# Kernel tuning notes

Measured on AMD Instinct MI355X. Metric: run time of the kernel, lower is better.

The kernel has to match this reference:

```python
import jax, jax.numpy as jnp
import numpy as np

B, T, D, U = 32, 2048, 512, 512


def setup_inputs() -> dict:
    key = jax.random.key(0)
    ks = jax.random.split(key, 6)
    value = jax.random.normal(ks[0], (B, T, D), dtype=jnp.float32)
    query = jax.random.normal(ks[1], (B, D), dtype=jnp.float32)
    mask = jax.random.randint(ks[2], (B, T), 0, 2, dtype=jnp.int32)
    # Glorot-ish scaled dense weights (no bias, matching Dense(use_bias=False))
    W1 = jax.random.normal(ks[3], (D, U), dtype=jnp.float32) * (1.0 / np.sqrt(D))
    W2 = jax.random.normal(ks[4], (D, U), dtype=jnp.float32) * (1.0 / np.sqrt(D))
    V = jax.random.normal(ks[5], (U,), dtype=jnp.float32) * (1.0 / np.sqrt(U))
    return {"value": value, "query": query, "mask": mask, "W1": W1, "W2": W2, "V": V}


def reference(value, query, mask, W1, W2, V):
    # Additive (Bahdanau) attention scores: u[b,t] = V . tanh(value[b,t] @ W1 + query[b] @ W2)
    w1_key = jnp.einsum('btd,du->btu', value, W1)          # [B, T, U]
    w2_query = jnp.einsum('bd,du->bu', query, W2)          # [B, U]
    u = jnp.einsum('btu,u->bt', jnp.tanh(w1_key + w2_query[:, None, :]), V)  # [B, T]
    # Masking: add -1e20 where mask == 0 (same as keras reference)
    u = u + (1.0 - mask.astype(u.dtype)) * jnp.asarray(-1e20, dtype=u.dtype)
    a = jax.nn.softmax(u, axis=1)                          # [B, T]
    # Pointer extraction: gather value row at argmax of attention weights
    idx = jnp.argmax(a, axis=1)                            # [B]
    context = jnp.take_along_axis(value, idx[:, None, None], axis=1)[:, 0, :]  # [B, D]
    return (context, a)
```

## Files before the change

### kernel.cpp

```cpp
#include <hip/hip_runtime.h>
#include <hip/hip_bf16.h>
#include <hip/hip_fp16.h>
#include <stdint.h>

#define B_ 32
#define T_ 2048
#define D_ 512
#define U_ 512
#define M_ (B_ * T_)

#define BM 64
#define BK 32
#define SAW 520
#define MAXC 4

typedef _Float16 half8  __attribute__((ext_vector_type(8)));
typedef float   floatx4 __attribute__((ext_vector_type(4)));

__device__ __forceinline__ float tanh_fast(float x) {
    float ax = fabsf(x);
    float e  = __expf(2.0f * ax);
    float t  = 1.0f - 2.0f / (e + 1.0f);
    return copysignf(t, x);
}

__device__ __forceinline__ void gld_lds16(const void* gsrc, void* lds_dst) {
    typedef __attribute__((address_space(1))) const char gch;
    typedef __attribute__((address_space(3))) char lch;
    __builtin_amdgcn_global_load_lds((const gch*)(uintptr_t)gsrc,
                                     (lch*)(uint32_t)(uintptr_t)lds_dst,
                                     16, 0, 0);
}

__global__ __launch_bounds__(256)
void k_prep(const float* __restrict__ W1, const float* __restrict__ query,
            const float* __restrict__ W2, _Float16* __restrict__ W1T,
            float* __restrict__ w2q) {
    const int bid = blockIdx.x;
    const int tid = threadIdx.x;
    if (bid < 64) {
        __shared__ float tile[64][65];
        const int bx = bid & 7;
        const int by = bid >> 3;
        const int k0 = bx * 64, n0 = by * 64;
        const int tx = tid & 63;
        const int ty = tid >> 6;
#pragma unroll
        for (int i = 0; i < 16; ++i) {
            int r = ty * 16 + i;
            tile[r][tx] = W1[(size_t)(k0 + r) * U_ + n0 + tx];
        }
        __syncthreads();
#pragma unroll
        for (int i = 0; i < 16; ++i) {
            int r = ty * 16 + i;
            W1T[(size_t)(n0 + r) * D_ + k0 + tx] = (_Float16)tile[tx][r];
        }
    } else {
        __shared__ float sq[D_];
        __shared__ float part[128];
        const int id = bid - 64;
        const int b  = id >> 2;
        const int nq = id & 3;
        sq[tid]       = query[b * D_ + tid];
        sq[tid + 256] = query[b * D_ + tid + 256];
        __syncthreads();
        const int n  = nq * 128 + (tid & 127);
        const int dh = tid >> 7;
        float acc = 0.f;
        const int d0 = dh * 256;
#pragma unroll 16
        for (int d = d0; d < d0 + 256; ++d)
            acc = fmaf(sq[d], W2[(size_t)d * U_ + n], acc);
        if (dh == 1) part[tid & 127] = acc;
        __syncthreads();
        if (dh == 0) w2q[b * U_ + n] = acc + part[tid];
    }
}

__global__ __launch_bounds__(512)
void k_gemm_u(const float* __restrict__ value,
              const _Float16* __restrict__ W1T,
              const float* __restrict__ w2q,
              const float* __restrict__ Vv,
              float* __restrict__ u_out) {
    __shared__ __align__(16) _Float16 sA[BM * SAW];
    __shared__ __align__(16) _Float16 sB[2][U_ * BK];
    __shared__ float sW2q[U_];
    __shared__ float sV[U_];
    __shared__ float sRed[8][BM];

    const int tid  = threadIdx.x;
    const int wave = tid >> 6;
    const int lane = tid & 63;
    const int l15  = lane & 15;
    const int lg   = lane >> 4;
    const int m0   = blockIdx.x * BM;
    const int b    = m0 >> 11;

    sW2q[tid] = w2q[b * U_ + tid];
    sV[tid]   = Vv[tid];

    const int bn  = lane >> 2;
    const int bk8 = (lane & 3) * 8;

#pragma unroll
    for (int jj = 0; jj < 4; ++jj) {
        const int inst = wave * 4 + jj;
        const int n = inst * 16 + bn;
        gld_lds16(W1T + (size_t)n * D_ + bk8, (void*)(&sB[0][inst * 512]));
    }

#pragma unroll
    for (int j = 0; j < 8; ++j) {
        const int row = wave * 8 + j;
        const float* src = value + (size_t)(m0 + row) * D_ + lane * 8;
        const floatx4 x0 = *(const floatx4*)(src);
        const floatx4 x1 = *(const floatx4*)(src + 4);
        half8 h;
        h[0] = (_Float16)x0[0]; h[1] = (_Float16)x0[1];
        h[2] = (_Float16)x0[2]; h[3] = (_Float16)x0[3];
        h[4] = (_Float16)x1[0]; h[5] = (_Float16)x1[1];
        h[6] = (_Float16)x1[2]; h[7] = (_Float16)x1[3];
        *(half8*)(&sA[row * SAW + lane * 8]) = h;
    }

    floatx4 acc[4][4];
    const floatx4 zero4 = {0.f, 0.f, 0.f, 0.f};
#pragma unroll
    for (int i = 0; i < 4; ++i)
#pragma unroll
        for (int j = 0; j < 4; ++j) acc[i][j] = zero4;

    __syncthreads();

    for (int kk = 0; kk < 16; ++kk) {
        const int cur = kk & 1;
        if (kk < 15) {
            const int k0n = (kk + 1) * BK;
#pragma unroll
            for (int jj = 0; jj < 4; ++jj) {
                const int inst = wave * 4 + jj;
                const int n = inst * 16 + bn;
                gld_lds16(W1T + (size_t)n * D_ + k0n + bk8,
                          (void*)(&sB[cur ^ 1][inst * 512]));
            }
        }
        half8 af[4], bf[4];
#pragma unroll
        for (int mi = 0; mi < 4; ++mi)
            af[mi] = *(const half8*)(&sA[(mi * 16 + l15) * SAW + kk * BK + lg * 8]);
#pragma unroll
        for (int ni = 0; ni < 4; ++ni) {
            const int n = wave * 64 + ni * 16 + l15;
            bf[ni] = *(const half8*)(&sB[cur][n * BK + lg * 8]);
        }
#pragma unroll
        for (int ni = 0; ni < 4; ++ni)
#pragma unroll
            for (int mi = 0; mi < 4; ++mi)
                acc[mi][ni] = __builtin_amdgcn_mfma_f32_16x16x32_f16(
                    af[mi], bf[ni], acc[mi][ni], 0, 0, 0);
        __syncthreads();
    }

    float ps[4][4];
#pragma unroll
    for (int mi = 0; mi < 4; ++mi)
#pragma unroll
        for (int j = 0; j < 4; ++j) ps[mi][j] = 0.f;

#pragma unroll
    for (int ni = 0; ni < 4; ++ni) {
        const int n = wave * 64 + ni * 16 + l15;
        const float w2 = sW2q[n];
        const float vv = sV[n];
#pragma unroll
        for (int mi = 0; mi < 4; ++mi)
#pragma unroll
            for (int j = 0; j < 4; ++j)
                ps[mi][j] += vv * tanh_fast(acc[mi][ni][j] + w2);
    }
#pragma unroll
    for (int off = 1; off < 16; off <<= 1)
#pragma unroll
        for (int mi = 0; mi < 4; ++mi)
#pragma unroll
            for (int j = 0; j < 4; ++j)
                ps[mi][j] += __shfl_xor(ps[mi][j], off, 64);

    if (l15 == 0) {
#pragma unroll
        for (int mi = 0; mi < 4; ++mi)
#pragma unroll
            for (int j = 0; j < 4; ++j)
                sRed[wave][mi * 16 + lg * 4 + j] = ps[mi][j];
    }
    __syncthreads();
    if (tid < BM) {
        float s = 0.f;
#pragma unroll
        for (int w = 0; w < 8; ++w) s += sRed[w][tid];
        u_out[m0 + tid] = s;
    }
}

__global__ __launch_bounds__(256)
void k_post(const float* __restrict__ u, const int* __restrict__ mask,
            const float* __restrict__ value, const float* __restrict__ W1,
            const float* __restrict__ w2q, const float* __restrict__ Vv,
            float* __restrict__ a_out, float* __restrict__ ctx_out) {
    __shared__ float sx[T_];
    __shared__ float rv[4];
    __shared__ int   ri[4];
    __shared__ float s_scalar;
    __shared__ int   s_cand[MAXC];
    __shared__ float s_score[MAXC];
    __shared__ __align__(16) float vrows[MAXC][D_];
    __shared__ int   s_t;

    const int b = blockIdx.x;
    const int tid = threadIdx.x;
    const int wave = tid >> 6, lane = tid & 63;

#pragma unroll
    for (int i = 0; i < 8; ++i) {
        const int t = tid * 8 + i;
        float x = u[b * T_ + t];
        if (mask[b * T_ + t] == 0) x = -1e20f;
        sx[t] = x;
    }
    __syncthreads();

    for (int r = 0; r < MAXC; ++r) {
        float v = -INFINITY; int vi = 0;
#pragma unroll
        for (int i = 0; i < 8; ++i) {
            const int t = tid * 8 + i;
            const float x = sx[t];
            if (x > v) { v = x; vi = t; }
        }
        for (int off = 32; off > 0; off >>= 1) {
            const float ov = __shfl_down(v, off, 64);
            const int   oi = __shfl_down(vi, off, 64);
            if (ov > v || (ov == v && oi < vi)) { v = ov; vi = oi; }
        }
        if (lane == 0) { rv[wave] = v; ri[wave] = vi; }
        __syncthreads();
        if (tid == 0) {
            float bv = rv[0]; int bi = ri[0];
            for (int w = 1; w < 4; ++w)
                if (rv[w] > bv || (rv[w] == bv && ri[w] < bi)) { bv = rv[w]; bi = ri[w]; }
            s_cand[r] = bi;
            if (r == 0) s_scalar = bv;
            sx[bi] = -INFINITY;
        }
        __syncthreads();
    }
    const float mx = s_scalar;

    float zloc = 0.f;
    float evals[8];
#pragma unroll
    for (int i = 0; i < 8; ++i) {
        const int t = tid * 8 + i;
        float x = u[b * T_ + t];
        if (mask[b * T_ + t] == 0) x = -1e20f;
        const float e = __expf(x - mx);
        evals[i] = e;
        zloc += e;
    }
    for (int off = 32; off > 0; off >>= 1) zloc += __shfl_down(zloc, off, 64);
    if (lane == 0) rv[wave] = zloc;
    __syncthreads();
    if (tid == 0) s_scalar = 1.0f / (rv[0] + rv[1] + rv[2] + rv[3]);
    __syncthreads();
    const float rz = s_scalar;
#pragma unroll
    for (int i = 0; i < 8; ++i) {
        const int t = tid * 8 + i;
        a_out[b * T_ + t] = evals[i] * rz;
    }

#pragma unroll
    for (int ci = 0; ci < MAXC; ++ci) {
        const int t = s_cand[ci];
        vrows[ci][tid]       = value[((size_t)b * T_ + t) * D_ + tid];
        vrows[ci][tid + 256] = value[((size_t)b * T_ + t) * D_ + tid + 256];
    }
    __syncthreads();

    float dots[2][MAXC];
#pragma unroll
    for (int j = 0; j < 2; ++j)
#pragma unroll
        for (int ci = 0; ci < MAXC; ++ci) dots[j][ci] = 0.f;

    for (int d4 = 0; d4 < D_; d4 += 4) {
        floatx4 vr[MAXC];
#pragma unroll
        for (int ci = 0; ci < MAXC; ++ci)
            vr[ci] = *(const floatx4*)(&vrows[ci][d4]);
#pragma unroll
        for (int k = 0; k < 4; ++k) {
            const float w0 = W1[(size_t)(d4 + k) * U_ + tid];
            const float w1 = W1[(size_t)(d4 + k) * U_ + tid + 256];
#pragma unroll
            for (int ci = 0; ci < MAXC; ++ci) {
                dots[0][ci] = fmaf(vr[ci][k], w0, dots[0][ci]);
                dots[1][ci] = fmaf(vr[ci][k], w1, dots[1][ci]);
            }
        }
    }
    float sc[MAXC];
#pragma unroll
    for (int ci = 0; ci < MAXC; ++ci) {
        const float n0v = Vv[tid]       * tanhf(dots[0][ci] + w2q[b * U_ + tid]);
        const float n1v = Vv[tid + 256] * tanhf(dots[1][ci] + w2q[b * U_ + tid + 256]);
        sc[ci] = n0v + n1v;
    }
#pragma unroll
    for (int ci = 0; ci < MAXC; ++ci)
        for (int off = 32; off > 0; off >>= 1)
            sc[ci] += __shfl_down(sc[ci], off, 64);
    if (lane == 0) {
#pragma unroll
        for (int ci = 0; ci < MAXC; ++ci) rv[ci * 0 + ci] = 0.f;
    }
    __syncthreads();
    if (lane == 0) {
#pragma unroll
        for (int ci = 0; ci < MAXC; ++ci)
            vrows[ci][wave] = sc[ci];
    }
    __syncthreads();
    if (tid == 0) {
#pragma unroll
        for (int ci = 0; ci < MAXC; ++ci) {
            const int t = s_cand[ci];
            float s = vrows[ci][0] + vrows[ci][1] + vrows[ci][2] + vrows[ci][3];
            if (mask[b * T_ + t] == 0) s = -1e20f;
            s_score[ci] = s;
        }
        float bv = s_score[0]; int bt = s_cand[0];
        for (int i = 1; i < MAXC; ++i) {
            if (s_score[i] > bv || (s_score[i] == bv && s_cand[i] < bt)) {
                bv = s_score[i]; bt = s_cand[i];
            }
        }
        s_t = bt;
    }
    __syncthreads();

    const int t = s_t;
    ctx_out[b * D_ + tid]       = value[((size_t)b * T_ + t) * D_ + tid];
    ctx_out[b * D_ + tid + 256] = value[((size_t)b * T_ + t) * D_ + tid + 256];
}

extern "C" void kernel_launch(void* const* d_in, const int* in_sizes, int n_in,
                              void* d_out, int out_size, void* d_ws, size_t ws_size,
                              hipStream_t stream) {
    const float* value = (const float*)d_in[0];
    const float* query = (const float*)d_in[1];
    const int*   mask  = (const int*)d_in[2];
    const float* W1    = (const float*)d_in[3];
    const float* W2    = (const float*)d_in[4];
    const float* Vv    = (const float*)d_in[5];

    char* ws = (char*)d_ws;
    _Float16* W1T  = (_Float16*)ws;
    float*    w2q  = (float*)(ws + 524288);
    float*    u_ws = (float*)(ws + 524288 + 65536);

    float* ctx_out = (float*)d_out;
    float* a_out   = (float*)d_out + B_ * D_;

    hipLaunchKernelGGL(k_prep,   dim3(192), dim3(256), 0, stream,
                       W1, query, W2, W1T, w2q);
    hipLaunchKernelGGL(k_gemm_u, dim3(M_ / BM), dim3(512), 0, stream,
                       value, W1T, w2q, Vv, u_ws);
    hipLaunchKernelGGL(k_post,   dim3(32), dim3(256), 0, stream,
                       u_ws, mask, value, W1, w2q, Vv, a_out, ctx_out);
}
```

Baseline: 306.9 us.

## Stream A tile per K-step with register prefetch and shrink LDS footprint

The GEMM kernel no longer converts the whole 64x512 value tile to fp16 in LDS up front. It now keeps a double-buffered 64x32 A slice, prefetching fp32 rows two K-steps ahead into registers and converting them after the MFMAs. This cuts LDS use from about 66KB to about 44KB, which allows higher occupancy (launch bounds now ask for 4 blocks), and overlaps the global loads of value with compute. The W1T LDS load mapping is also changed to a contiguous per-lane layout, and the w2q/V values are read directly from global memory instead of being staged in LDS. An unused rv write is removed.

```diff
diff --git a/kernel.cpp b/kernel.cpp
--- a/kernel.cpp
+++ b/kernel.cpp
@@ -11,10 +11,11 @@
 
 #define BM 64
 #define BK 32
-#define SAW 520
+#define SAW 40
 #define MAXC 4
 
 typedef _Float16 half8  __attribute__((ext_vector_type(8)));
+typedef _Float16 half4_t __attribute__((ext_vector_type(4)));
 typedef float   floatx4 __attribute__((ext_vector_type(4)));
 
 __device__ __forceinline__ float tanh_fast(float x) {
@@ -78,16 +79,14 @@
     }
 }
 
-__global__ __launch_bounds__(512)
+__global__ __launch_bounds__(512, 4)
 void k_gemm_u(const float* __restrict__ value,
               const _Float16* __restrict__ W1T,
               const float* __restrict__ w2q,
               const float* __restrict__ Vv,
               float* __restrict__ u_out) {
-    __shared__ __align__(16) _Float16 sA[BM * SAW];
+    __shared__ __align__(16) _Float16 sA[2][BM * SAW];
     __shared__ __align__(16) _Float16 sB[2][U_ * BK];
-    __shared__ float sW2q[U_];
-    __shared__ float sV[U_];
     __shared__ float sRed[8][BM];
 
     const int tid  = threadIdx.x;
@@ -98,31 +97,28 @@
     const int m0   = blockIdx.x * BM;
     const int b    = m0 >> 11;
 
-    sW2q[tid] = w2q[b * U_ + tid];
-    sV[tid]   = Vv[tid];
-
-    const int bn  = lane >> 2;
-    const int bk8 = (lane & 3) * 8;
-
+    const int bnl  = l15;
+    const int bhi8 = lg * 8;
+
+    const int ar = tid >> 3;
+    const int ac = (tid & 7) * 4;
+    const float* aptr = value + (size_t)(m0 + ar) * D_ + ac;
+
+    floatx4 rA[2];
+
+    rA[0] = *(const floatx4*)(aptr);
+    rA[1] = *(const floatx4*)(aptr + BK);
 #pragma unroll
     for (int jj = 0; jj < 4; ++jj) {
         const int inst = wave * 4 + jj;
-        const int n = inst * 16 + bn;
-        gld_lds16(W1T + (size_t)n * D_ + bk8, (void*)(&sB[0][inst * 512]));
-    }
-
-#pragma unroll
-    for (int j = 0; j < 8; ++j) {
-        const int row = wave * 8 + j;
-        const float* src = value + (size_t)(m0 + row) * D_ + lane * 8;
-        const floatx4 x0 = *(const floatx4*)(src);
-        const floatx4 x1 = *(const floatx4*)(src + 4);
-        half8 h;
-        h[0] = (_Float16)x0[0]; h[1] = (_Float16)x0[1];
-        h[2] = (_Float16)x0[2]; h[3] = (_Float16)x0[3];
-        h[4] = (_Float16)x1[0]; h[5] = (_Float16)x1[1];
-        h[6] = (_Float16)x1[2]; h[7] = (_Float16)x1[3];
-        *(half8*)(&sA[row * SAW + lane * 8]) = h;
+        const int n = inst * 16 + bnl;
+        gld_lds16(W1T + (size_t)n * D_ + bhi8, (void*)(&sB[0][inst * 512]));
+    }
+    {
+        half4_t h;
+        h[0] = (_Float16)rA[0][0]; h[1] = (_Float16)rA[0][1];
+        h[2] = (_Float16)rA[0][2]; h[3] = (_Float16)rA[0][3];
+        *(half4_t*)(&sA[0][ar * SAW + ac]) = h;
     }
 
     floatx4 acc[4][4];
@@ -141,19 +137,21 @@
 #pragma unroll
             for (int jj = 0; jj < 4; ++jj) {
                 const int inst = wave * 4 + jj;
-                const int n = inst * 16 + bn;
-                gld_lds16(W1T + (size_t)n * D_ + k0n + bk8,
+                const int n = inst * 16 + bnl;
+                gld_lds16(W1T + (size_t)n * D_ + k0n + bhi8,
                           (void*)(&sB[cur ^ 1][inst * 512]));
             }
         }
+        if (kk < 14) rA[cur] = *(const floatx4*)(aptr + (kk + 2) * BK);
+
         half8 af[4], bf[4];
 #pragma unroll
         for (int mi = 0; mi < 4; ++mi)
-            af[mi] = *(const half8*)(&sA[(mi * 16 + l15) * SAW + kk * BK + lg * 8]);
+            af[mi] = *(const half8*)(&sA[cur][(mi * 16 + l15) * SAW + lg * 8]);
 #pragma unroll
         for (int ni = 0; ni < 4; ++ni) {
-            const int n = wave * 64 + ni * 16 + l15;
-            bf[ni] = *(const half8*)(&sB[cur][n * BK + lg * 8]);
+            const int inst = wave * 4 + ni;
+            bf[ni] = *(const half8*)(&sB[cur][inst * 512 + (lg * 16 + l15) * 8]);
         }
 #pragma unroll
         for (int ni = 0; ni < 4; ++ni)
@@ -161,6 +159,14 @@
             for (int mi = 0; mi < 4; ++mi)
                 acc[mi][ni] = __builtin_amdgcn_mfma_f32_16x16x32_f16(
                     af[mi], bf[ni], acc[mi][ni], 0, 0, 0);
+
+        if (kk < 15) {
+            const floatx4 v4 = rA[cur ^ 1];
+            half4_t h;
+            h[0] = (_Float16)v4[0]; h[1] = (_Float16)v4[1];
+            h[2] = (_Float16)v4[2]; h[3] = (_Float16)v4[3];
+            *(half4_t*)(&sA[cur ^ 1][ar * SAW + ac]) = h;
+        }
         __syncthreads();
     }
 
@@ -173,8 +179,8 @@
 #pragma unroll
     for (int ni = 0; ni < 4; ++ni) {
         const int n = wave * 64 + ni * 16 + l15;
-        const float w2 = sW2q[n];
-        const float vv = sV[n];
+        const float w2 = w2q[b * U_ + n];
+        const float vv = Vv[n];
 #pragma unroll
         for (int mi = 0; mi < 4; ++mi)
 #pragma unroll
@@ -323,10 +329,6 @@
     for (int ci = 0; ci < MAXC; ++ci)
         for (int off = 32; off > 0; off >>= 1)
             sc[ci] += __shfl_down(sc[ci], off, 64);
-    if (lane == 0) {
-#pragma unroll
-        for (int ci = 0; ci < MAXC; ++ci) rv[ci * 0 + ci] = 0.f;
-    }
     __syncthreads();
     if (lane == 0) {
 #pragma unroll
```

Result: no change. 306.0 us (-0.3%).

## Keep W1 slice resident in registers and stream value rows through double-buffered LDS

Applied to the files above, without the earlier changes.

The GEMM kernel is restructured so that each block owns a 256-column slice of W1. The slice is held in registers as fp16 MFMA B operands, loaded straight from fp32 W1, which removes the transpose prep kernel and the per-k-step LDS staging of W1. Each block walks 256 value rows in chunks of 32, register-prefetched and double-buffered in LDS, and uses 32x32x16 MFMAs. It writes partial scores per column slice, which the post kernel sums. The risks are high register pressure (32 half8 registers per lane under a 2-blocks-per-SM launch bound), a strided uncoalesced initial W1 load, and value being read twice, once per column slice.

```diff
diff --git a/kernel.cpp b/kernel.cpp
--- a/kernel.cpp
+++ b/kernel.cpp
@@ -1,5 +1,4 @@
 #include <hip/hip_runtime.h>
-#include <hip/hip_bf16.h>
 #include <hip/hip_fp16.h>
 #include <stdint.h>
 
@@ -9,13 +8,17 @@
 #define U_ 512
 #define M_ (B_ * T_)
 
-#define BM 64
-#define BK 32
+#define NSPLIT 2
+#define NCOLS 256
+#define CHUNK 32
+#define NCHUNK 8
+#define ROWS_PB 256
 #define SAW 520
 #define MAXC 4
 
-typedef _Float16 half8  __attribute__((ext_vector_type(8)));
-typedef float   floatx4 __attribute__((ext_vector_type(4)));
+typedef _Float16 half8   __attribute__((ext_vector_type(8)));
+typedef float   floatx4  __attribute__((ext_vector_type(4)));
+typedef float   floatx16 __attribute__((ext_vector_type(16)));
 
 __device__ __forceinline__ float tanh_fast(float x) {
     float ax = fabsf(x);
@@ -24,189 +27,138 @@
     return copysignf(t, x);
 }
 
-__device__ __forceinline__ void gld_lds16(const void* gsrc, void* lds_dst) {
-    typedef __attribute__((address_space(1))) const char gch;
-    typedef __attribute__((address_space(3))) char lch;
-    __builtin_amdgcn_global_load_lds((const gch*)(uintptr_t)gsrc,
-                                     (lch*)(uint32_t)(uintptr_t)lds_dst,
-                                     16, 0, 0);
-}
-
 __global__ __launch_bounds__(256)
-void k_prep(const float* __restrict__ W1, const float* __restrict__ query,
-            const float* __restrict__ W2, _Float16* __restrict__ W1T,
-            float* __restrict__ w2q) {
-    const int bid = blockIdx.x;
+void k_w2q(const float* __restrict__ query, const float* __restrict__ W2,
+           float* __restrict__ w2q) {
+    __shared__ float sq[D_];
+    __shared__ float part[128];
     const int tid = threadIdx.x;
-    if (bid < 64) {
-        __shared__ float tile[64][65];
-        const int bx = bid & 7;
-        const int by = bid >> 3;
-        const int k0 = bx * 64, n0 = by * 64;
-        const int tx = tid & 63;
-        const int ty = tid >> 6;
-#pragma unroll
-        for (int i = 0; i < 16; ++i) {
-            int r = ty * 16 + i;
-            tile[r][tx] = W1[(size_t)(k0 + r) * U_ + n0 + tx];
-        }
-        __syncthreads();
-#pragma unroll
-        for (int i = 0; i < 16; ++i) {
-            int r = ty * 16 + i;
-            W1T[(size_t)(n0 + r) * D_ + k0 + tx] = (_Float16)tile[tx][r];
-        }
-    } else {
-        __shared__ float sq[D_];
-        __shared__ float part[128];
-        const int id = bid - 64;
-        const int b  = id >> 2;
-        const int nq = id & 3;
-        sq[tid]       = query[b * D_ + tid];
-        sq[tid + 256] = query[b * D_ + tid + 256];
-        __syncthreads();
-        const int n  = nq * 128 + (tid & 127);
-        const int dh = tid >> 7;
-        float acc = 0.f;
-        const int d0 = dh * 256;
+    const int b  = blockIdx.x >> 2;
+    const int nq = blockIdx.x & 3;
+    sq[tid]       = query[b * D_ + tid];
+    sq[tid + 256] = query[b * D_ + tid + 256];
+    __syncthreads();
+    const int n  = nq * 128 + (tid & 127);
+    const int dh = tid >> 7;
+    float acc = 0.f;
+    const int d0 = dh * 256;
 #pragma unroll 16
-        for (int d = d0; d < d0 + 256; ++d)
-            acc = fmaf(sq[d], W2[(size_t)d * U_ + n], acc);
-        if (dh == 1) part[tid & 127] = acc;
-        __syncthreads();
-        if (dh == 0) w2q[b * U_ + n] = acc + part[tid];
-    }
-}
-
-__global__ __launch_bounds__(512)
+    for (int d = d0; d < d0 + 256; ++d)
+        acc = fmaf(sq[d], W2[(size_t)d * U_ + n], acc);
+    if (dh == 1) part[tid & 127] = acc;
+    __syncthreads();
+    if (dh == 0) w2q[b * U_ + n] = acc + part[tid];
+}
+
+__global__ __launch_bounds__(512, 2)
 void k_gemm_u(const float* __restrict__ value,
-              const _Float16* __restrict__ W1T,
+              const float* __restrict__ W1,
               const float* __restrict__ w2q,
               const float* __restrict__ Vv,
-              float* __restrict__ u_out) {
-    __shared__ __align__(16) _Float16 sA[BM * SAW];
-    __shared__ __align__(16) _Float16 sB[2][U_ * BK];
-    __shared__ float sW2q[U_];
-    __shared__ float sV[U_];
-    __shared__ float sRed[8][BM];
+              float* __restrict__ u_part) {
+    __shared__ __align__(16) _Float16 sA[2][CHUNK * SAW];
+    __shared__ float sRed[2][8][CHUNK];
 
     const int tid  = threadIdx.x;
     const int wave = tid >> 6;
     const int lane = tid & 63;
-    const int l15  = lane & 15;
-    const int lg   = lane >> 4;
-    const int m0   = blockIdx.x * BM;
-    const int b    = m0 >> 11;
-
-    sW2q[tid] = w2q[b * U_ + tid];
-    sV[tid]   = Vv[tid];
-
-    const int bn  = lane >> 2;
-    const int bk8 = (lane & 3) * 8;
-
-#pragma unroll
-    for (int jj = 0; jj < 4; ++jj) {
-        const int inst = wave * 4 + jj;
-        const int n = inst * 16 + bn;
-        gld_lds16(W1T + (size_t)n * D_ + bk8, (void*)(&sB[0][inst * 512]));
-    }
-
-#pragma unroll
-    for (int j = 0; j < 8; ++j) {
-        const int row = wave * 8 + j;
-        const float* src = value + (size_t)(m0 + row) * D_ + lane * 8;
-        const floatx4 x0 = *(const floatx4*)(src);
-        const floatx4 x1 = *(const floatx4*)(src + 4);
+    const int l31  = lane & 31;
+    const int hi   = lane >> 5;
+    const int slice = blockIdx.x & 1;
+    const int mblk  = blockIdx.x >> 1;
+    const int mbase = mblk * ROWS_PB;
+    const int b     = mbase >> 11;
+
+    const int n_g = slice * NCOLS + wave * 32 + l31;
+    const float w2 = w2q[b * U_ + n_g];
+    const float vv = Vv[n_g];
+
+    half8 breg[32];
+#pragma unroll
+    for (int s = 0; s < 32; ++s) {
+        const int k0 = s * 16 + hi * 8;
         half8 h;
-        h[0] = (_Float16)x0[0]; h[1] = (_Float16)x0[1];
-        h[2] = (_Float16)x0[2]; h[3] = (_Float16)x0[3];
-        h[4] = (_Float16)x1[0]; h[5] = (_Float16)x1[1];
-        h[6] = (_Float16)x1[2]; h[7] = (_Float16)x1[3];
-        *(half8*)(&sA[row * SAW + lane * 8]) = h;
-    }
-
-    floatx4 acc[4][4];
-    const floatx4 zero4 = {0.f, 0.f, 0.f, 0.f};
-#pragma unroll
-    for (int i = 0; i < 4; ++i)
-#pragma unroll
-        for (int j = 0; j < 4; ++j) acc[i][j] = zero4;
-
-    __syncthreads();
-
-    for (int kk = 0; kk < 16; ++kk) {
-        const int cur = kk & 1;
-        if (kk < 15) {
-            const int k0n = (kk + 1) * BK;
-#pragma unroll
-            for (int jj = 0; jj < 4; ++jj) {
-                const int inst = wave * 4 + jj;
-                const int n = inst * 16 + bn;
-                gld_lds16(W1T + (size_t)n * D_ + k0n + bk8,
-                          (void*)(&sB[cur ^ 1][inst * 512]));
+#pragma unroll
+        for (int j = 0; j < 8; ++j)
+            h[j] = (_Float16)W1[(size_t)(k0 + j) * U_ + n_g];
+        breg[s] = h;
+    }
+
+    floatx4 rA[8];
+
+#define A_ISSUE(c)                                                              \
+    {                                                                           \
+        _Pragma("unroll")                                                       \
+        for (int i = 0; i < 4; ++i) {                                           \
+            const float* p = value +                                            \
+                (size_t)(mbase + (c) * CHUNK + i * 8 + wave) * D_ + lane * 8;   \
+            rA[i * 2]     = *(const floatx4*)p;                                 \
+            rA[i * 2 + 1] = *(const floatx4*)(p + 4);                           \
+        }                                                                       \
+    }
+
+#define A_STORE(buf)                                                            \
+    {                                                                           \
+        _Pragma("unroll")                                                       \
+        for (int i = 0; i < 4; ++i) {                                           \
+            half8 h;                                                            \
+            _Pragma("unroll")                                                   \
+            for (int j = 0; j < 4; ++j) {                                       \
+                h[j]     = (_Float16)rA[i * 2][j];                              \
+                h[4 + j] = (_Float16)rA[i * 2 + 1][j];                          \
+            }                                                                   \
+            *(half8*)(&sA[buf][(i * 8 + wave) * SAW + lane * 8]) = h;           \
+        }                                                                       \
+    }
+
+    A_ISSUE(0);
+    A_STORE(0);
+    A_ISSUE(1);
+    __syncthreads();
+
+    for (int c = 0; c < NCHUNK; ++c) {
+        const int cur = c & 1;
+        if (c + 1 < NCHUNK) A_STORE(cur ^ 1);
+        if (c + 2 < NCHUNK) A_ISSUE(c + 2);
+
+        floatx16 acc;
+#pragma unroll
+        for (int r = 0; r < 16; ++r) acc[r] = 0.f;
+
+#pragma unroll
+        for (int s = 0; s < 32; ++s) {
+            const half8 af = *(const half8*)(&sA[cur][l31 * SAW + s * 16 + hi * 8]);
+            acc = __builtin_amdgcn_mfma_f32_32x32x16_f16(af, breg[s], acc, 0, 0, 0);
+        }
+
+        float ps[16];
+#pragma unroll
+        for (int r = 0; r < 16; ++r) ps[r] = vv * tanh_fast(acc[r] + w2);
+#pragma unroll
+        for (int off = 1; off < 32; off <<= 1)
+#pragma unroll
+            for (int r = 0; r < 16; ++r) ps[r] += __shfl_xor(ps[r], off, 64);
+        if (l31 == 0) {
+#pragma unroll
+            for (int r = 0; r < 16; ++r) {
+                const int row = (r & 3) + 8 * (r >> 2) + 4 * hi;
+                sRed[cur][wave][row] = ps[r];
             }
         }
-        half8 af[4], bf[4];
-#pragma unroll
-        for (int mi = 0; mi < 4; ++mi)
-            af[mi] = *(const half8*)(&sA[(mi * 16 + l15) * SAW + kk * BK + lg * 8]);
-#pragma unroll
-        for (int ni = 0; ni < 4; ++ni) {
-            const int n = wave * 64 + ni * 16 + l15;
-            bf[ni] = *(const half8*)(&sB[cur][n * BK + lg * 8]);
-        }
-#pragma unroll
-        for (int ni = 0; ni < 4; ++ni)
-#pragma unroll
-            for (int mi = 0; mi < 4; ++mi)
-                acc[mi][ni] = __builtin_amdgcn_mfma_f32_16x16x32_f16(
-                    af[mi], bf[ni], acc[mi][ni], 0, 0, 0);
         __syncthreads();
-    }
-
-    float ps[4][4];
-#pragma unroll
-    for (int mi = 0; mi < 4; ++mi)
-#pragma unroll
-        for (int j = 0; j < 4; ++j) ps[mi][j] = 0.f;
-
-#pragma unroll
-    for (int ni = 0; ni < 4; ++ni) {
-        const int n = wave * 64 + ni * 16 + l15;
-        const float w2 = sW2q[n];
-        const float vv = sV[n];
-#pragma unroll
-        for (int mi = 0; mi < 4; ++mi)
-#pragma unroll
-            for (int j = 0; j < 4; ++j)
-                ps[mi][j] += vv * tanh_fast(acc[mi][ni][j] + w2);
-    }
-#pragma unroll
-    for (int off = 1; off < 16; off <<= 1)
-#pragma unroll
-        for (int mi = 0; mi < 4; ++mi)
-#pragma unroll
-            for (int j = 0; j < 4; ++j)
-                ps[mi][j] += __shfl_xor(ps[mi][j], off, 64);
-
-    if (l15 == 0) {
-#pragma unroll
-        for (int mi = 0; mi < 4; ++mi)
-#pragma unroll
-            for (int j = 0; j < 4; ++j)
-                sRed[wave][mi * 16 + lg * 4 + j] = ps[mi][j];
-    }
-    __syncthreads();
-    if (tid < BM) {
-        float s = 0.f;
-#pragma unroll
-        for (int w = 0; w < 8; ++w) s += sRed[w][tid];
-        u_out[m0 + tid] = s;
-    }
+        if (tid < CHUNK) {
+            float ssum = 0.f;
+#pragma unroll
+            for (int w = 0; w < 8; ++w) ssum += sRed[cur][w][tid];
+            u_part[(size_t)slice * M_ + mbase + c * CHUNK + tid] = ssum;
+        }
+    }
+#undef A_ISSUE
+#undef A_STORE
 }
 
 __global__ __launch_bounds__(256)
-void k_post(const float* __restrict__ u, const int* __restrict__ mask,
+void k_post(const float* __restrict__ u_part, const int* __restrict__ mask,
             const float* __restrict__ value, const float* __restrict__ W1,
             const float* __restrict__ w2q, const float* __restrict__ Vv,
             float* __restrict__ a_out, float* __restrict__ ctx_out) {
@@ -226,7 +178,7 @@
 #pragma unroll
     for (int i = 0; i < 8; ++i) {
         const int t = tid * 8 + i;
-        float x = u[b * T_ + t];
+        float x = u_part[b * T_ + t] + u_part[M_ + b * T_ + t];
         if (mask[b * T_ + t] == 0) x = -1e20f;
         sx[t] = x;
     }
@@ -264,7 +216,7 @@
 #pragma unroll
     for (int i = 0; i < 8; ++i) {
         const int t = tid * 8 + i;
-        float x = u[b * T_ + t];
+        float x = u_part[b * T_ + t] + u_part[M_ + b * T_ + t];
         if (mask[b * T_ + t] == 0) x = -1e20f;
         const float e = __expf(x - mx);
         evals[i] = e;
@@ -323,10 +275,6 @@
     for (int ci = 0; ci < MAXC; ++ci)
         for (int off = 32; off > 0; off >>= 1)
             sc[ci] += __shfl_down(sc[ci], off, 64);
-    if (lane == 0) {
-#pragma unroll
-        for (int ci = 0; ci < MAXC; ++ci) rv[ci * 0 + ci] = 0.f;
-    }
     __syncthreads();
     if (lane == 0) {
 #pragma unroll
@@ -368,17 +316,15 @@
     const float* Vv    = (const float*)d_in[5];
 
     char* ws = (char*)d_ws;
-    _Float16* W1T  = (_Float16*)ws;
-    float*    w2q  = (float*)(ws + 524288);
-    float*    u_ws = (float*)(ws + 524288 + 65536);
+    float* w2q    = (float*)ws;
+    float* u_part = (float*)(ws + 65536);
 
     float* ctx_out = (float*)d_out;
     float* a_out   = (float*)d_out + B_ * D_;
 
-    hipLaunchKernelGGL(k_prep,   dim3(192), dim3(256), 0, stream,
-                       W1, query, W2, W1T, w2q);
-    hipLaunchKernelGGL(k_gemm_u, dim3(M_ / BM), dim3(512), 0, stream,
-                       value, W1T, w2q, Vv, u_ws);
+    hipLaunchKernelGGL(k_w2q,    dim3(128), dim3(256), 0, stream, query, W2, w2q);
+    hipLaunchKernelGGL(k_gemm_u, dim3(NSPLIT * (M_ / ROWS_PB)), dim3(512), 0, stream,
+                       value, W1, w2q, Vv, u_part);
     hipLaunchKernelGGL(k_post,   dim3(32), dim3(256), 0, stream,
-                       u_ws, mask, value, W1, w2q, Vv, a_out, ctx_out);
-}
+                       u_part, mask, value, W1, w2q, Vv, a_out, ctx_out);
+}
```

New measurement: 292.4 us. -4.7%, faster.
